# Kernel optimization log

Hardware: AMD Instinct MI355X
Metric: run time of the kernel (lower is better)

## Reference

```python
import jax, jax.numpy as jnp
import numpy as np

V = 50288; D = 768; L = 12; SPLIT = 6; L_LORA = L - SPLIT
NSTATE = 64; HDIM = 64
DIN = 2 * D                         # expand=2 -> 1536
H = DIN // HDIM                     # 24 heads
K = 4                               # depthwise conv kernel
DPROJ = 2 * DIN + 2 * NSTATE + H    # 3224
CONVD = DIN + 2 * NSTATE            # 1664
R = 8; LORA_SCALE = 2.0             # alpha/rank = 2r/r
EPS = 1e-5


def _rms(x, w):
    return x * jax.lax.rsqrt(jnp.mean(x * x, axis=-1, keepdims=True) + EPS) * w


def _ssm_scan(dt, A, Bm, Cm, xh):
    # dt:[B,T,H]  A:[H]  Bm,Cm:[B,T,N]  xh:[B,T,H,P]
    dA = jnp.exp(dt * A)
    def step(h, inp):
        dA_t, dt_t, B_t, C_t, x_t = inp
        h = dA_t[:, :, None, None] * h + (dt_t[..., None] * x_t)[..., None] * B_t[:, None, None, :]
        return h, jnp.einsum('bhpn,bn->bhp', h, C_t)
    h0 = jnp.zeros((dt.shape[0], H, HDIM, NSTATE), dt.dtype)
    xs = tuple(jnp.moveaxis(a, 1, 0) for a in (dA, dt, Bm, Cm, xh))
    _, ys = jax.lax.scan(step, h0, xs)
    return jnp.moveaxis(ys, 0, 1)  # [B,T,H,P]


@jax.checkpoint
def _mixer(u, in_w, cw, cb, dtb, A_log, Dsk, gw, out_w):
    # Mamba2 selective-scan block (ngroups=1, no biases on projections)
    Bsz, T, _ = u.shape
    zxbcdt = u @ in_w.T                              # [B,T,DPROJ]
    z = zxbcdt[..., :DIN]
    xBC = zxbcdt[..., DIN:DIN + CONVD]
    dt = zxbcdt[..., DIN + CONVD:]
    xp = jnp.pad(xBC, ((0, 0), (K - 1, 0), (0, 0)))  # causal depthwise conv1d
    xBC = jax.nn.silu(cb + sum(cw[:, k] * xp[:, k:k + T] for k in range(K)))
    xh = xBC[..., :DIN].reshape(Bsz, T, H, HDIM)
    Bm = xBC[..., DIN:DIN + NSTATE]
    Cm = xBC[..., DIN + NSTATE:]
    dt = jax.nn.softplus(dt + dtb)
    y = _ssm_scan(dt, -jnp.exp(A_log), Bm, Cm, xh) + Dsk[None, None, :, None] * xh
    y = _rms(y.reshape(Bsz, T, DIN) * jax.nn.silu(z), gw)   # gated RMSNorm
    return y @ out_w.T


def _run_base(x, res, p):
    def step(carry, q):
        x, res = carry
        res = x + res
        h = _mixer(_rms(res, q['nw']), q['iw'], q['cw'], q['cb'], q['dtb'],
                   q['al'], q['dk'], q['gw'], q['ow'])
        return (h, res), None
    (x, res), _ = jax.lax.scan(step, (x, res), p)
    return x, res


def _run_lora(x, res, p):
    def step(carry, q):
        x, res = carry
        res = x + res
        iw = q['iw'] + LORA_SCALE * (q['ibw'] @ q['iaw'])   # LoRALinear effective weight
        ow = q['ow'] + LORA_SCALE * (q['obw'] @ q['oaw'])
        h = _mixer(_rms(res, q['nw']), iw, q['cw'], q['cb'], q['dtb'],
                   q['al'], q['dk'], q['gw'], ow)
        return (h, res), None
    (x, res), _ = jax.lax.scan(step, (x, res), p)
    return x, res


def _rope(x, loop_i):
    # LoopRoPE: rotate interleaved pairs of hidden dims by angle theta_i * loop_i
    inv_freq = 1.0 / (10000.0 ** (jnp.arange(0, D, 2, dtype=jnp.float32) / D))
    f = loop_i * inv_freq
    cos_v = jnp.repeat(jnp.cos(f), 2)
    sin_v = jnp.repeat(jnp.sin(f), 2)
    x1, x2 = x[..., ::2], x[..., 1::2]
    rot = jnp.stack([-x2, x1], axis=-1).reshape(x.shape)
    return x * cos_v + rot * sin_v


def _forward(input_ids, n_loops, embedding, norm_w, in_w, conv_w, conv_b, dt_bias, A_log,
             D_skip, gnorm_w, out_w, lora_in_A, lora_in_B, lora_out_A, lora_out_B,
             core_in_w, core_conv_w, core_conv_b, core_dt_bias, core_A_log, core_D,
             core_gnorm_w, core_out_w, loop_norm_w, lifeline_gate, norm_f_w, lm_head_w):
    base = {'nw': norm_w[:SPLIT], 'iw': in_w[:SPLIT], 'cw': conv_w[:SPLIT], 'cb': conv_b[:SPLIT],
            'dtb': dt_bias[:SPLIT], 'al': A_log[:SPLIT], 'dk': D_skip[:SPLIT],
            'gw': gnorm_w[:SPLIT], 'ow': out_w[:SPLIT]}
    lora = {'nw': norm_w[SPLIT:], 'iw': in_w[SPLIT:], 'cw': conv_w[SPLIT:], 'cb': conv_b[SPLIT:],
            'dtb': dt_bias[SPLIT:], 'al': A_log[SPLIT:], 'dk': D_skip[SPLIT:],
            'gw': gnorm_w[SPLIT:], 'ow': out_w[SPLIT:],
            'iaw': lora_in_A, 'ibw': lora_in_B, 'oaw': lora_out_A, 'obw': lora_out_B}
    x = embedding[input_ids]                       # [B,T,D]
    res = jnp.zeros_like(x)                        # residual=None -> zeros
    x, res = _run_base(x, res, base)               # frozen layers [0:6]
    x, res = _run_lora(x, res, lora)               # LoRA layers [6:12]
    x_prompt = jax.lax.stop_gradient(x)            # x.clone().detach()
    for i in range(int(n_loops)):
        x = x + lifeline_gate * x_prompt           # lifeline injection
        x = _rope(x, float(i))                     # loop-index RoPE
        x, res = _run_lora(x, res, lora)           # run_lora recursion body
        x = x + _mixer(x, core_in_w, core_conv_w, core_conv_b, core_dt_bias,
                       core_A_log, core_D, core_gnorm_w, core_out_w)  # mamba2_core
        x = _rms(x, loop_norm_w)                   # loop_norm
    h = _rms(x + res, norm_f_w)                    # norm_f(x, residual, prenorm=False)
    return h @ lm_head_w.T                         # lm_head logits [B,T,V]


def setup_inputs() -> dict:
    key = jax.random.key(0)
    ks = iter(jax.random.split(key, 64))
    f32 = jnp.float32
    def w(shape, s=0.02):
        return (s * jax.random.normal(next(ks), shape)).astype(f32)
    inp = {
        'input_ids': jax.random.randint(next(ks), (2, 512), 0, 50277, dtype=jnp.int32),
        'n_loops': 3,
        'embedding': w((V, D)),
        'norm_w': jnp.ones((L, D), f32),
        'in_w': w((L, DPROJ, D)),
        'conv_w': w((L, CONVD, K), 0.2),
        'conv_b': jnp.zeros((L, CONVD), f32),
        'dt_bias': w((L, H), 0.5),
        'A_log': jnp.log(1.0 + 15.0 * jax.random.uniform(next(ks), (L, H))).astype(f32),
        'D_skip': jnp.ones((L, H), f32),
        'gnorm_w': jnp.ones((L, DIN), f32),
        'out_w': w((L, D, DIN)),
        'lora_in_A': w((L_LORA, R, D), 0.05),
        'lora_in_B': w((L_LORA, DPROJ, R), 0.05),
        'lora_out_A': w((L_LORA, R, DIN), 0.05),
        'lora_out_B': w((L_LORA, D, R), 0.05),
        'core_in_w': w((DPROJ, D)),
        'core_conv_w': w((CONVD, K), 0.2),
        'core_conv_b': jnp.zeros((CONVD,), f32),
        'core_dt_bias': w((H,), 0.5),
        'core_A_log': jnp.log(1.0 + 15.0 * jax.random.uniform(next(ks), (H,))).astype(f32),
        'core_D': jnp.ones((H,), f32),
        'core_gnorm_w': jnp.ones((DIN,), f32),
        'core_out_w': w((D, DIN)),
        'loop_norm_w': jnp.ones((D,), f32),
        'lifeline_gate': jnp.ones((D,), f32),
        'norm_f_w': jnp.ones((D,), f32),
        'lm_head_w': w((V, D)),
    }
    return inp


def reference(input_ids, n_loops, embedding, norm_w, in_w, conv_w, conv_b, dt_bias, A_log,
              D_skip, gnorm_w, out_w, lora_in_A, lora_in_B, lora_out_A, lora_out_B,
              core_in_w, core_conv_w, core_conv_b, core_dt_bias, core_A_log, core_D,
              core_gnorm_w, core_out_w, loop_norm_w, lifeline_gate, norm_f_w, lm_head_w):
    return _forward(input_ids, n_loops, embedding, norm_w, in_w, conv_w, conv_b, dt_bias,
                    A_log, D_skip, gnorm_w, out_w, lora_in_A, lora_in_B, lora_out_A,
                    lora_out_B, core_in_w, core_conv_w, core_conv_b, core_dt_bias,
                    core_A_log, core_D, core_gnorm_w, core_out_w, loop_norm_w,
                    lifeline_gate, norm_f_w, lm_head_w)
```

## Files before the change

kernel.cpp:

```cpp
#include <hip/hip_runtime.h>
#include <math.h>

constexpr int Bsz   = 2;
constexpr int Tseq  = 512;
constexpr int Mtok  = Bsz * Tseq;
constexpr int Dm    = 768;
constexpr int DINc  = 1536;
constexpr int Hn    = 24;
constexpr int NS    = 64;
constexpr int KC    = 4;
constexpr int DPROJc = 2*DINc + 2*NS + Hn;
constexpr int CONVDc = DINc + 2*NS;
constexpr int NL    = 12;
constexpr int SPL   = 6;
constexpr int LLO   = 6;
constexpr int NCH   = 8;
constexpr int Vv    = 50288;
constexpr float EPSc = 1e-5f;
constexpr int NLOOPS = 3;

#define DEVI __device__ __forceinline__

typedef _Float16 f16x8 __attribute__((ext_vector_type(8)));
typedef float    f32x4 __attribute__((ext_vector_type(4)));

DEVI float siluf(float x){ return x / (1.0f + expf(-x)); }
DEVI float softplusf(float x){ return (x > 20.0f) ? x : log1pf(expf(x)); }
DEVI unsigned short f2h(float f){
  union { _Float16 h; unsigned short u; } c;
  c.h = (_Float16)f;
  return c.u;
}
DEVI float h2f(unsigned short u){
  union { unsigned short u; _Float16 h; } c;
  c.u = u; return (float)c.h;
}

DEVI void gload16(const void* g, void* l){
  __builtin_amdgcn_global_load_lds(
      (const __attribute__((address_space(1))) void*)g,
      (__attribute__((address_space(3))) void*)l, 16, 0, 0);
}

DEVI float blk_reduce256(float v, float* sh){
  #pragma unroll
  for (int o = 32; o; o >>= 1) v += __shfl_down(v, o);
  int lane = threadIdx.x & 63, w = threadIdx.x >> 6;
  if (lane == 0) sh[w] = v;
  __syncthreads();
  return sh[0] + sh[1] + sh[2] + sh[3];
}

__global__ void k_embed(const int* __restrict__ ids, const float* __restrict__ emb,
                        float* __restrict__ x){
  int m = blockIdx.x;
  int id = ids[m];
  const float4* src = (const float4*)(emb + (size_t)id * Dm);
  float4* dst = (float4*)(x + (size_t)m * Dm);
  int i = threadIdx.x;
  dst[i] = src[i];
}

__global__ void k_f2h(const float* __restrict__ in, unsigned short* __restrict__ out, int n4){
  int e = blockIdx.x*256 + threadIdx.x;
  if (e >= n4) return;
  float4 v = ((const float4*)in)[e];
  ushort4 o; o.x=f2h(v.x); o.y=f2h(v.y); o.z=f2h(v.z); o.w=f2h(v.w);
  ((ushort4*)out)[e] = o;
}

__global__ __launch_bounds__(256) void k_addrms(const float* __restrict__ xin,
    float* __restrict__ res, unsigned short* __restrict__ ub,
    const float* __restrict__ w){
  int m = blockIdx.x, tid = threadIdx.x;
  __shared__ float sh[4];
  const float* xr = xin + (size_t)m*Dm;
  float* rr = res + (size_t)m*Dm;
  float r[3]; float ss = 0.f;
  #pragma unroll
  for (int k=0;k<3;k++){ int e = tid + k*256; float v = xr[e] + rr[e]; r[k]=v; ss += v*v; }
  ss = blk_reduce256(ss, sh);
  float rs = 1.0f / sqrtf(ss/(float)Dm + EPSc);
  #pragma unroll
  for (int k=0;k<3;k++){
    int e = tid + k*256;
    rr[e] = r[k];
    ub[(size_t)m*Dm+e] = f2h(r[k]*rs*w[e]);
  }
}

__global__ __launch_bounds__(256) void k_addrms_p(const float* __restrict__ part,
    float* __restrict__ res, unsigned short* __restrict__ ub,
    const float* __restrict__ w){
  int m = blockIdx.x, tid = threadIdx.x;
  __shared__ float sh[4];
  const size_t tot = (size_t)Mtok*Dm;
  float* rr = res + (size_t)m*Dm;
  float r[3]; float ss = 0.f;
  #pragma unroll
  for (int k=0;k<3;k++){
    int e = tid + k*256;
    size_t idx = (size_t)m*Dm + e;
    float v = rr[e] + part[idx] + part[tot+idx] + part[2*tot+idx] + part[3*tot+idx];
    r[k]=v; ss += v*v;
  }
  ss = blk_reduce256(ss, sh);
  float rs = 1.0f / sqrtf(ss/(float)Dm + EPSc);
  #pragma unroll
  for (int k=0;k<3;k++){
    int e = tid + k*256;
    rr[e] = r[k];
    ub[(size_t)m*Dm+e] = f2h(r[k]*rs*w[e]);
  }
}

__global__ void k_sum_xp(const float* __restrict__ part, float* __restrict__ x,
                         float* __restrict__ xp){
  size_t e = (size_t)blockIdx.x*256 + threadIdx.x;
  const size_t tot = (size_t)Mtok*Dm;
  if (e >= tot) return;
  float v = part[e] + part[tot+e] + part[2*tot+e] + part[3*tot+e];
  x[e] = v; xp[e] = v;
}

__global__ void k_f2h_sum(const float* __restrict__ part, float* __restrict__ x,
                          unsigned short* __restrict__ ub){
  size_t e = (size_t)blockIdx.x*256 + threadIdx.x;
  const size_t tot = (size_t)Mtok*Dm;
  if (e >= tot) return;
  float v = part[e] + part[tot+e] + part[2*tot+e] + part[3*tot+e];
  x[e] = v; ub[e] = f2h(v);
}

__global__ __launch_bounds__(256) void k_rms_p(const float* __restrict__ part,
    float* __restrict__ x, const float* __restrict__ w){
  int m = blockIdx.x, tid = threadIdx.x;
  __shared__ float sh[4];
  const size_t tot = (size_t)Mtok*Dm;
  float* xr = x + (size_t)m*Dm;
  float r[3]; float ss = 0.f;
  #pragma unroll
  for (int k=0;k<3;k++){
    int e = tid + k*256;
    size_t idx = (size_t)m*Dm + e;
    float v = xr[e] + part[idx] + part[tot+idx] + part[2*tot+idx] + part[3*tot+idx];
    r[k]=v; ss += v*v;
  }
  ss = blk_reduce256(ss, sh);
  float rs = 1.0f / sqrtf(ss/(float)Dm + EPSc);
  #pragma unroll
  for (int k=0;k<3;k++){ int e = tid + k*256; xr[e] = r[k]*rs*w[e]; }
}

__global__ __launch_bounds__(128) void k_liferope(float* __restrict__ x,
    const float* __restrict__ xp, const float* __restrict__ gate, float iF){
  int m = blockIdx.x, tid = threadIdx.x;
  float* xr = x + (size_t)m*Dm;
  const float* pr = xp + (size_t)m*Dm;
  #pragma unroll
  for (int k=0;k<3;k++){
    int j = tid + k*128;
    int d0 = 2*j, d1 = d0+1;
    float v0 = xr[d0] + gate[d0]*pr[d0];
    float v1 = xr[d1] + gate[d1]*pr[d1];
    float invf = expf(-9.210340371976184f * ((float)(2*j) * (1.0f/768.0f)));
    float f = iF * invf;
    float cv = cosf(f), sv = sinf(f);
    xr[d0] = v0*cv - v1*sv;
    xr[d1] = v1*cv + v0*sv;
  }
}

__global__ __launch_bounds__(256) void k_gemm_h(
    const unsigned short* __restrict__ A,
    const unsigned short* __restrict__ Bw,
    void* __restrict__ Cv, int Nd, int Kd, int outmode){
  alignas(16) __shared__ unsigned short lA[2][128*64];
  alignas(16) __shared__ unsigned short lB[2][128*64];
  const int tid  = threadIdx.x;
  const int lane = tid & 63;
  const int wv   = tid >> 6;
  const int wm   = wv >> 1, wn = wv & 1;
  const int gx = gridDim.x, gy = gridDim.y;
  const int nwg = gx*gy;
  const int flat = blockIdx.x + gx*blockIdx.y;
  const int q = nwg >> 3, r = nwg & 7;
  const int xcd = flat & 7, pos = flat >> 3;
  const int lg = (xcd < r ? xcd*(q+1) : r*(q+1) + (xcd - r)*q) + pos;
  const int m_idx = lg % gy, n_idx = lg / gy;
  const int n0 = n_idx * 128;
  const int m0 = m_idx * 128;
  const int KS = gridDim.z;
  const int kchunk = Kd / KS;
  const int kbeg = blockIdx.z * kchunk;
  const int nsteps = kchunk / 64;

  f32x4 acc[4][4] = {};

  auto stage = [&](int buf, int k0){
    #pragma unroll
    for (int i=0;i<4;i++){
      int seg = tid + i*256;
      int row = seg >> 3;
      int c8  = (seg & 7) ^ (row & 7);
      gload16(A + (size_t)(m0 + row)*Kd + k0 + c8*8, &lA[buf][seg*8]);
      int rn = n0 + row; rn = (rn < Nd) ? rn : (Nd - 1);
      gload16(Bw + (size_t)rn*Kd + k0 + c8*8, &lB[buf][seg*8]);
    }
  };

  stage(0, kbeg);
  for (int t=0; t<nsteps; ++t){
    const int cur = t & 1;
    if (t+1 < nsteps){
      stage(cur^1, kbeg + (t+1)*64);
      __builtin_amdgcn_sched_barrier(0);
      asm volatile("s_waitcnt vmcnt(8)" ::: "memory");
    } else {
      asm volatile("s_waitcnt vmcnt(0)" ::: "memory");
    }
    __builtin_amdgcn_s_barrier();
    __builtin_amdgcn_sched_barrier(0);
    #pragma unroll
    for (int kk=0; kk<2; kk++){
      f16x8 af[4], bfr[4];
      #pragma unroll
      for (int f=0; f<4; f++){
        int rowa = wm*64 + f*16 + (lane & 15);
        int ba = rowa*128 + ((kk*64 + (lane>>4)*16) ^ ((rowa & 7) << 4));
        af[f] = *(const f16x8*)((const char*)&lA[cur][0] + ba);
        int rowb = wn*64 + f*16 + (lane & 15);
        int bb = rowb*128 + ((kk*64 + (lane>>4)*16) ^ ((rowb & 7) << 4));
        bfr[f] = *(const f16x8*)((const char*)&lB[cur][0] + bb);
      }
      #pragma unroll
      for (int fm=0; fm<4; fm++)
        #pragma unroll
        for (int fn=0; fn<4; fn++)
          acc[fm][fn] = __builtin_amdgcn_mfma_f32_16x16x32_f16(af[fm], bfr[fn], acc[fm][fn], 0, 0, 0);
    }
    __builtin_amdgcn_s_barrier();
  }

  #pragma unroll
  for (int fm=0; fm<4; fm++){
    int mbase = m0 + wm*64 + fm*16 + ((lane>>4)<<2);
    #pragma unroll
    for (int fn=0; fn<4; fn++){
      int n = n0 + wn*64 + fn*16 + (lane & 15);
      if (n < Nd){
        #pragma unroll
        for (int rr=0;rr<4;rr++){
          size_t idx = (size_t)(mbase + rr)*Nd + n;
          float v = acc[fm][fn][rr];
          if (outmode == 0){
            float* Cb = (float*)Cv + (size_t)blockIdx.z*((size_t)Mtok*Nd);
            Cb[idx] = v;
          } else if (outmode == 1){
            ((float*)Cv)[idx] = v;
          } else {
            ((unsigned short*)Cv)[idx] = f2h(v);
          }
        }
      }
    }
  }
}

__global__ void k_prep_in(const float* __restrict__ W12, const float* __restrict__ Wc,
    const float* __restrict__ lA, const float* __restrict__ lB,
    unsigned short* __restrict__ out){
  const int tot4 = DPROJc*Dm/4;
  int e4 = blockIdx.x*256 + threadIdx.x;
  if (e4 >= tot4) return;
  int l = blockIdx.y;
  const float* W = (l < 12) ? W12 + (size_t)l*DPROJc*Dm : Wc;
  const int k4n = Dm/4;
  int n = e4 / k4n, k4 = e4 - n*k4n;
  float4 wv = *(const float4*)(W + (size_t)n*Dm + k4*4);
  float s0=wv.x, s1=wv.y, s2=wv.z, s3=wv.w;
  if (l >= SPL && l < 12){
    int ll = l - SPL;
    const float* Bl = lB + (size_t)ll*DPROJc*8;
    const float* Al = lA + (size_t)ll*8*Dm;
    #pragma unroll
    for (int r=0;r<8;r++){
      float b = 2.0f * Bl[n*8+r];
      float4 a = *(const float4*)(Al + (size_t)r*Dm + k4*4);
      s0 += b*a.x; s1 += b*a.y; s2 += b*a.z; s3 += b*a.w;
    }
  }
  ushort4 o; o.x=f2h(s0); o.y=f2h(s1); o.z=f2h(s2); o.w=f2h(s3);
  ((ushort4*)(out + (size_t)l*DPROJc*Dm))[e4] = o;
}

__global__ void k_prep_out(const float* __restrict__ W12, const float* __restrict__ Wc,
    const float* __restrict__ lA, const float* __restrict__ lB,
    unsigned short* __restrict__ out){
  const int tot4 = Dm*DINc/4;
  int e4 = blockIdx.x*256 + threadIdx.x;
  if (e4 >= tot4) return;
  int l = blockIdx.y;
  const float* W = (l < 12) ? W12 + (size_t)l*Dm*DINc : Wc;
  const int k4n = DINc/4;
  int n = e4 / k4n, k4 = e4 - n*k4n;
  float4 wv = *(const float4*)(W + (size_t)n*DINc + k4*4);
  float s0=wv.x, s1=wv.y, s2=wv.z, s3=wv.w;
  if (l >= SPL && l < 12){
    int ll = l - SPL;
    const float* Bl = lB + (size_t)ll*Dm*8;
    const float* Al = lA + (size_t)ll*8*DINc;
    #pragma unroll
    for (int r=0;r<8;r++){
      float b = 2.0f * Bl[n*8+r];
      float4 a = *(const float4*)(Al + (size_t)r*DINc + k4*4);
      s0 += b*a.x; s1 += b*a.y; s2 += b*a.z; s3 += b*a.w;
    }
  }
  ushort4 o; o.x=f2h(s0); o.y=f2h(s1); o.z=f2h(s2); o.w=f2h(s3);
  ((ushort4*)(out + (size_t)l*Dm*DINc))[e4] = o;
}

DEVI f16x8 ldfrag(const unsigned short (*T)[72], int row, int k0){
  return *(const f16x8*)&T[row][k0];
}

__global__ __launch_bounds__(256) void k_s1(const unsigned short* __restrict__ zxh,
    const float* __restrict__ cw, const float* __restrict__ cb,
    const float* __restrict__ dtb, const float* __restrict__ alog,
    float* __restrict__ S, float* __restrict__ ctot){
  int bh = blockIdx.x; int b = bh / Hn, h = bh % Hn; int c = blockIdx.y;
  __shared__ unsigned short XT[64][72];
  __shared__ unsigned short BwT[64][72];
  __shared__ float wv[64];
  int tid = threadIdx.x;
  int base_m = b*Tseq + c*64;
  if (tid < 64){
    float Av = -expf(alog[h]);
    float zdt = h2f(zxh[(size_t)(base_m+tid)*DPROJc + DINc + CONVDc + h]) + dtb[h];
    float dt = softplusf(zdt);
    float s = dt * Av;
    #pragma unroll
    for (int o=1;o<64;o<<=1){ float v = __shfl_up(s, o); if (tid >= o) s += v; }
    if (tid == 63) ctot[bh*NCH + c] = s;
    float ce = __shfl(s, 63);
    wv[tid] = expf(ce - s) * dt;
  }
  __syncthreads();
  int ch = tid & 63;
  int t0 = (tid >> 6) * 16;
  int tl = c*64 + t0;
  {
    int cc = h*64 + ch;
    float4 w4 = *(const float4*)&cw[cc*KC];
    float bias = cb[cc];
    const unsigned short* zp = zxh + (size_t)base_m*DPROJc + DINc + cc;
    float v0 = (tl >= 3) ? h2f(zp[(long)(t0-3)*DPROJc]) : 0.f;
    float v1 = (tl >= 2) ? h2f(zp[(long)(t0-2)*DPROJc]) : 0.f;
    float v2 = (tl >= 1) ? h2f(zp[(long)(t0-1)*DPROJc]) : 0.f;
    #pragma unroll
    for (int i=0;i<16;i++){
      float v3 = h2f(zp[(long)(t0+i)*DPROJc]);
      float o = bias + w4.x*v0 + w4.y*v1 + w4.z*v2 + w4.w*v3;
      XT[ch][t0+i] = f2h(siluf(o));
      v0=v1; v1=v2; v2=v3;
    }
  }
  {
    int cc = DINc + ch;
    float4 w4 = *(const float4*)&cw[cc*KC];
    float bias = cb[cc];
    const unsigned short* zp = zxh + (size_t)base_m*DPROJc + DINc + cc;
    float v0 = (tl >= 3) ? h2f(zp[(long)(t0-3)*DPROJc]) : 0.f;
    float v1 = (tl >= 2) ? h2f(zp[(long)(t0-2)*DPROJc]) : 0.f;
    float v2 = (tl >= 1) ? h2f(zp[(long)(t0-1)*DPROJc]) : 0.f;
    #pragma unroll
    for (int i=0;i<16;i++){
      float v3 = h2f(zp[(long)(t0+i)*DPROJc]);
      float o = bias + w4.x*v0 + w4.y*v1 + w4.z*v2 + w4.w*v3;
      BwT[ch][t0+i] = f2h(siluf(o) * wv[t0+i]);
      v0=v1; v1=v2; v2=v3;
    }
  }
  __syncthreads();
  int lane = tid & 63, wid = tid >> 6, wmp = wid >> 1, wnn = wid & 1;
  f32x4 acc[2][2] = {};
  #pragma unroll
  for (int kk=0; kk<2; kk++){
    int k0 = kk*32 + (lane>>4)*8;
    f16x8 a[2], bf[2];
    #pragma unroll
    for (int f=0; f<2; f++){
      a[f]  = ldfrag(XT,  wmp*32 + f*16 + (lane&15), k0);
      bf[f] = ldfrag(BwT, wnn*32 + f*16 + (lane&15), k0);
    }
    #pragma unroll
    for (int fm=0; fm<2; fm++)
      #pragma unroll
      for (int fn=0; fn<2; fn++)
        acc[fm][fn] = __builtin_amdgcn_mfma_f32_16x16x32_f16(a[fm], bf[fn], acc[fm][fn], 0, 0, 0);
  }
  float* Sb = S + ((size_t)(bh*NCH + c))*4096;
  #pragma unroll
  for (int fm=0; fm<2; fm++)
    #pragma unroll
    for (int fn=0; fn<2; fn++)
      #pragma unroll
      for (int rg=0; rg<4; rg++){
        int p = wmp*32 + fm*16 + ((lane>>4)<<2) + rg;
        int n = wnn*32 + fn*16 + (lane&15);
        Sb[p*64 + n] = acc[fm][fn][rg];
      }
}

__global__ void k_s2(const float* __restrict__ S, const float* __restrict__ ctot,
                     float* __restrict__ hst){
  int gid = blockIdx.x*256 + threadIdx.x;
  int bh = gid >> 12; int e = gid & 4095;
  float hv = 0.f;
  #pragma unroll
  for (int c=0;c<NCH;c++){
    size_t idx = ((size_t)(bh*NCH + c))*4096 + e;
    hst[idx] = hv;
    float Ac = expf(ctot[bh*NCH + c]);
    hv = Ac*hv + S[idx];
  }
}

__global__ __launch_bounds__(256) void k_s3(const unsigned short* __restrict__ zxh,
    const float* __restrict__ cw, const float* __restrict__ cb,
    const float* __restrict__ dtb, const float* __restrict__ alog,
    const float* __restrict__ hst, const float* __restrict__ Dsk,
    unsigned short* __restrict__ y){
  int bh = blockIdx.x; int b = bh / Hn, h = bh % Hn; int c = blockIdx.y;
  __shared__ unsigned short Ch[64][72];
  __shared__ unsigned short Bh[64][72];
  __shared__ unsigned short XhT[64][72];
  __shared__ unsigned short hT[64][72];
  __shared__ unsigned short Mh[64][72];
  __shared__ float cumS[64], dtS[64];
  int tid = threadIdx.x;
  int base_m = b*Tseq + c*64;
  if (tid < 64){
    float Av = -expf(alog[h]);
    float zdt = h2f(zxh[(size_t)(base_m+tid)*DPROJc + DINc + CONVDc + h]) + dtb[h];
    float dt = softplusf(zdt);
    float s = dt * Av;
    #pragma unroll
    for (int o=1;o<64;o<<=1){ float v = __shfl_up(s, o); if (tid >= o) s += v; }
    cumS[tid] = s;
    dtS[tid]  = dt;
  }
  int ch = tid & 63;
  int t0 = (tid >> 6) * 16;
  int tl = c*64 + t0;
  {
    int cc = h*64 + ch;
    float4 w4 = *(const float4*)&cw[cc*KC];
    float bias = cb[cc];
    const unsigned short* zp = zxh + (size_t)base_m*DPROJc + DINc + cc;
    float v0 = (tl >= 3) ? h2f(zp[(long)(t0-3)*DPROJc]) : 0.f;
    float v1 = (tl >= 2) ? h2f(zp[(long)(t0-2)*DPROJc]) : 0.f;
    float v2 = (tl >= 1) ? h2f(zp[(long)(t0-1)*DPROJc]) : 0.f;
    #pragma unroll
    for (int i=0;i<16;i++){
      float v3 = h2f(zp[(long)(t0+i)*DPROJc]);
      float o = bias + w4.x*v0 + w4.y*v1 + w4.z*v2 + w4.w*v3;
      XhT[ch][t0+i] = f2h(siluf(o));
      v0=v1; v1=v2; v2=v3;
    }
  }
  {
    int cc = DINc + ch;
    float4 w4 = *(const float4*)&cw[cc*KC];
    float bias = cb[cc];
    const unsigned short* zp = zxh + (size_t)base_m*DPROJc + DINc + cc;
    float v0 = (tl >= 3) ? h2f(zp[(long)(t0-3)*DPROJc]) : 0.f;
    float v1 = (tl >= 2) ? h2f(zp[(long)(t0-2)*DPROJc]) : 0.f;
    float v2 = (tl >= 1) ? h2f(zp[(long)(t0-1)*DPROJc]) : 0.f;
    #pragma unroll
    for (int i=0;i<16;i++){
      float v3 = h2f(zp[(long)(t0+i)*DPROJc]);
      float o = bias + w4.x*v0 + w4.y*v1 + w4.z*v2 + w4.w*v3;
      Bh[t0+i][ch] = f2h(siluf(o));
      v0=v1; v1=v2; v2=v3;
    }
  }
  {
    int cc = DINc + NS + ch;
    float4 w4 = *(const float4*)&cw[cc*KC];
    float bias = cb[cc];
    const unsigned short* zp = zxh + (size_t)base_m*DPROJc + DINc + cc;
    float v0 = (tl >= 3) ? h2f(zp[(long)(t0-3)*DPROJc]) : 0.f;
    float v1 = (tl >= 2) ? h2f(zp[(long)(t0-2)*DPROJc]) : 0.f;
    float v2 = (tl >= 1) ? h2f(zp[(long)(t0-1)*DPROJc]) : 0.f;
    #pragma unroll
    for (int i=0;i<16;i++){
      float v3 = h2f(zp[(long)(t0+i)*DPROJc]);
      float o = bias + w4.x*v0 + w4.y*v1 + w4.z*v2 + w4.w*v3;
      Ch[t0+i][ch] = f2h(siluf(o));
      v0=v1; v1=v2; v2=v3;
    }
  }
  {
    const float* hb = hst + ((size_t)(bh*NCH + c))*4096;
    for (int e4 = tid; e4 < 1024; e4 += 256){
      float4 hv = ((const float4*)hb)[e4];
      int p = (e4 << 2) >> 6, n = (e4 << 2) & 63;
      ushort4 o; o.x=f2h(hv.x); o.y=f2h(hv.y); o.z=f2h(hv.z); o.w=f2h(hv.w);
      *(ushort4*)&hT[p][n] = o;
    }
  }
  __syncthreads();
  int lane = tid & 63, wid = tid >> 6, wmt = wid >> 1, wns = wid & 1;
  f32x4 g[2][2] = {};
  #pragma unroll
  for (int kk=0; kk<2; kk++){
    int k0 = kk*32 + (lane>>4)*8;
    f16x8 a[2], bf[2];
    #pragma unroll
    for (int f=0; f<2; f++){
      a[f]  = ldfrag(Ch, wmt*32 + f*16 + (lane&15), k0);
      bf[f] = ldfrag(Bh, wns*32 + f*16 + (lane&15), k0);
    }
    #pragma unroll
    for (int fm=0; fm<2; fm++)
      #pragma unroll
      for (int fn=0; fn<2; fn++)
        g[fm][fn] = __builtin_amdgcn_mfma_f32_16x16x32_f16(a[fm], bf[fn], g[fm][fn], 0, 0, 0);
  }
  #pragma unroll
  for (int fm=0; fm<2; fm++)
    #pragma unroll
    for (int fn=0; fn<2; fn++)
      #pragma unroll
      for (int rg=0; rg<4; rg++){
        int t = wmt*32 + fm*16 + ((lane>>4)<<2) + rg;
        int s = wns*32 + fn*16 + (lane&15);
        float val = (s <= t) ? expf(cumS[t] - cumS[s]) * dtS[s] * g[fm][fn][rg] : 0.f;
        Mh[t][s] = f2h(val);
      }
  __syncthreads();
  f32x4 aL[2][2] = {}, aS[2][2] = {};
  #pragma unroll
  for (int kk=0; kk<2; kk++){
    int k0 = kk*32 + (lane>>4)*8;
    f16x8 m_[2], x_[2], c_[2], h_[2];
    #pragma unroll
    for (int f=0; f<2; f++){
      m_[f] = ldfrag(Mh,  wmt*32 + f*16 + (lane&15), k0);
      x_[f] = ldfrag(XhT, wns*32 + f*16 + (lane&15), k0);
      c_[f] = ldfrag(Ch,  wmt*32 + f*16 + (lane&15), k0);
      h_[f] = ldfrag(hT,  wns*32 + f*16 + (lane&15), k0);
    }
    #pragma unroll
    for (int fm=0; fm<2; fm++)
      #pragma unroll
      for (int fn=0; fn<2; fn++){
        aL[fm][fn] = __builtin_amdgcn_mfma_f32_16x16x32_f16(m_[fm], x_[fn], aL[fm][fn], 0, 0, 0);
        aS[fm][fn] = __builtin_amdgcn_mfma_f32_16x16x32_f16(c_[fm], h_[fn], aS[fm][fn], 0, 0, 0);
      }
  }
  float Dh = Dsk[h];
  #pragma unroll
  for (int fm=0; fm<2; fm++)
    #pragma unroll
    for (int fn=0; fn<2; fn++)
      #pragma unroll
      for (int rg=0; rg<4; rg++){
        int t = wmt*32 + fm*16 + ((lane>>4)<<2) + rg;
        int p = wns*32 + fn*16 + (lane&15);
        float Pt = expf(cumS[t]);
        float xv = h2f(XhT[p][t]);
        float o = aL[fm][fn][rg] + Pt*aS[fm][fn][rg] + Dh*xv;
        y[(size_t)(base_m+t)*DINc + h*64 + p] = f2h(o);
      }
}

__global__ __launch_bounds__(256) void k_gate(const unsigned short* __restrict__ zxh,
    const unsigned short* __restrict__ y, unsigned short* __restrict__ yb,
    const float* __restrict__ gw){
  int m = blockIdx.x, tid = threadIdx.x;
  __shared__ float sh[4];
  const unsigned short* zr = zxh + (size_t)m*DPROJc;
  const unsigned short* yr = y + (size_t)m*DINc;
  float g[6]; float ss = 0.f;
  #pragma unroll
  for (int k=0;k<6;k++){
    int e = tid + k*256;
    float z = h2f(zr[e]);
    float v = h2f(yr[e]) * siluf(z);
    g[k] = v; ss += v*v;
  }
  ss = blk_reduce256(ss, sh);
  float rs = 1.0f / sqrtf(ss/(float)DINc + EPSc);
  #pragma unroll
  for (int k=0;k<6;k++){
    int e = tid + k*256;
    yb[(size_t)m*DINc + e] = f2h(g[k]*rs*gw[e]);
  }
}

struct WSP {
  float *x,*res,*xp,*ctot,*Sc,*hst,*part;
  unsigned short *zxh,*yh,*ub,*yb,*wib,*wob,*whb;
};

static void run_mixer_h(hipStream_t st, const WSP& w, const unsigned short* ub_in,
    const unsigned short* iw, const float* cw, const float* cb, const float* dtb,
    const float* al, const float* dk, const float* gw, const unsigned short* ow){
  dim3 gIn((DPROJc + 127)/128, Mtok/128, 1);
  k_gemm_h<<<gIn, 256, 0, st>>>(ub_in, iw, w.zxh, DPROJc, Dm, 2);
  k_s1<<<dim3(Bsz*Hn, NCH), 256, 0, st>>>(w.zxh, cw, cb, dtb, al, w.Sc, w.ctot);
  k_s2<<<(Bsz*Hn*4096)/256, 256, 0, st>>>(w.Sc, w.ctot, w.hst);
  k_s3<<<dim3(Bsz*Hn, NCH), 256, 0, st>>>(w.zxh, cw, cb, dtb, al, w.hst, dk, w.yh);
  k_gate<<<Mtok, 256, 0, st>>>(w.zxh, w.yh, w.yb, gw);
  dim3 gOut(Dm/128, Mtok/128, 4);
  k_gemm_h<<<gOut, 256, 0, st>>>(w.yb, ow, w.part, Dm, DINc, 0);
}

extern "C" void kernel_launch(void* const* d_in, const int* in_sizes, int n_in,
                              void* d_out, int out_size, void* d_ws, size_t ws_size,
                              hipStream_t stream){
  const int*   ids        = (const int*)  d_in[0];
  const float* emb        = (const float*)d_in[2];
  const float* norm_w     = (const float*)d_in[3];
  const float* in_w       = (const float*)d_in[4];
  const float* conv_w     = (const float*)d_in[5];
  const float* conv_b     = (const float*)d_in[6];
  const float* dt_bias    = (const float*)d_in[7];
  const float* A_log      = (const float*)d_in[8];
  const float* D_skip     = (const float*)d_in[9];
  const float* gnorm_w    = (const float*)d_in[10];
  const float* out_w      = (const float*)d_in[11];
  const float* lora_in_A  = (const float*)d_in[12];
  const float* lora_in_B  = (const float*)d_in[13];
  const float* lora_out_A = (const float*)d_in[14];
  const float* lora_out_B = (const float*)d_in[15];
  const float* core_in_w  = (const float*)d_in[16];
  const float* core_conv_w= (const float*)d_in[17];
  const float* core_conv_b= (const float*)d_in[18];
  const float* core_dtb   = (const float*)d_in[19];
  const float* core_A_log = (const float*)d_in[20];
  const float* core_D     = (const float*)d_in[21];
  const float* core_gw    = (const float*)d_in[22];
  const float* core_out_w = (const float*)d_in[23];
  const float* loop_norm_w= (const float*)d_in[24];
  const float* life_gate  = (const float*)d_in[25];
  const float* norm_f_w   = (const float*)d_in[26];
  const float* lm_head_w  = (const float*)d_in[27];
  (void)in_sizes; (void)n_in; (void)out_size; (void)ws_size;

  char* pb = (char*)d_ws;
  auto balloc = [&](size_t bytes){
    char* q = pb; pb += (bytes + 255) & ~(size_t)255; return q;
  };
  WSP w;
  w.x    = (float*)balloc((size_t)Mtok*Dm*4);
  w.res  = (float*)balloc((size_t)Mtok*Dm*4);
  w.xp   = (float*)balloc((size_t)Mtok*Dm*4);
  w.ctot = (float*)balloc((size_t)Bsz*Hn*NCH*4);
  w.Sc   = (float*)balloc((size_t)Bsz*Hn*NCH*4096*4);
  w.hst  = (float*)balloc((size_t)Bsz*Hn*NCH*4096*4);
  w.part = (float*)balloc((size_t)4*Mtok*Dm*4);
  w.zxh  = (unsigned short*)balloc((size_t)Mtok*DPROJc*2);
  w.yh   = (unsigned short*)balloc((size_t)Mtok*DINc*2);
  w.ub   = (unsigned short*)balloc((size_t)Mtok*Dm*2);
  w.yb   = (unsigned short*)balloc((size_t)Mtok*DINc*2);

  const size_t IWN = (size_t)DPROJc*Dm;
  const size_t OWN = (size_t)Dm*DINc;
  const size_t HWN = (size_t)Vv*Dm;
  w.wib = (unsigned short*)balloc(13*IWN*2);
  w.wob = (unsigned short*)balloc(13*OWN*2);
  w.whb = (unsigned short*)balloc(HWN*2);

  k_prep_in<<<dim3((IWN/4 + 255)/256, 13), 256, 0, stream>>>(
      in_w, core_in_w, lora_in_A, lora_in_B, w.wib);
  k_prep_out<<<dim3((OWN/4 + 255)/256, 13), 256, 0, stream>>>(
      out_w, core_out_w, lora_out_A, lora_out_B, w.wob);
  k_f2h<<<(HWN/4 + 255)/256, 256, 0, stream>>>(lm_head_w, w.whb, (int)(HWN/4));

  k_embed<<<Mtok, 192, 0, stream>>>(ids, emb, w.x);
  hipMemsetAsync(w.res, 0, (size_t)Mtok*Dm*sizeof(float), stream);

  const size_t totMD = (size_t)Mtok*Dm;

  auto mixer_l = [&](int l){
    run_mixer_h(stream, w, w.ub,
        w.wib + (size_t)l*IWN, conv_w + (size_t)l*CONVDc*KC, conv_b + (size_t)l*CONVDc,
        dt_bias + (size_t)l*Hn, A_log + (size_t)l*Hn, D_skip + (size_t)l*Hn,
        gnorm_w + (size_t)l*DINc, w.wob + (size_t)l*OWN);
  };
  k_addrms<<<Mtok, 256, 0, stream>>>(w.x, w.res, w.ub, norm_w);
  mixer_l(0);
  for (int l=1; l<NL; l++){
    k_addrms_p<<<Mtok, 256, 0, stream>>>(w.part, w.res, w.ub, norm_w + (size_t)l*Dm);
    mixer_l(l);
  }
  k_sum_xp<<<(totMD + 255)/256, 256, 0, stream>>>(w.part, w.x, w.xp);
  for (int i=0;i<NLOOPS;i++){
    k_liferope<<<Mtok, 128, 0, stream>>>(w.x, w.xp, life_gate, (float)i);
    k_addrms<<<Mtok, 256, 0, stream>>>(w.x, w.res, w.ub, norm_w + (size_t)SPL*Dm);
    mixer_l(SPL);
    for (int l=SPL+1; l<NL; l++){
      k_addrms_p<<<Mtok, 256, 0, stream>>>(w.part, w.res, w.ub, norm_w + (size_t)l*Dm);
      mixer_l(l);
    }
    k_f2h_sum<<<(totMD + 255)/256, 256, 0, stream>>>(w.part, w.x, w.ub);
    run_mixer_h(stream, w, w.ub,
        w.wib + 12*IWN, core_conv_w, core_conv_b, core_dtb, core_A_log, core_D,
        core_gw, w.wob + 12*OWN);
    k_rms_p<<<Mtok, 256, 0, stream>>>(w.part, w.x, loop_norm_w);
  }
  k_addrms<<<Mtok, 256, 0, stream>>>(w.x, w.res, w.ub, norm_f_w);
  dim3 gHead((Vv + 127)/128, Mtok/128, 1);
  k_gemm_h<<<gHead, 256, 0, stream>>>(w.ub, w.whb, d_out, Vv, Dm, 1);
}
```

Before: 2.752 ms.

## Fuse gated RMSNorm into scan epilogue and out-projection GEMM

Removes the separate gating and RMSNorm kernel from each mixer. The scan kernel now applies the silu(z) gate, writes the gated output and atomically accumulates per-row sums of squares. The out-projection GEMM reads those sums and applies the inverse RMS scale in its epilogue, and the norm weight is folded into the pre-converted out_w columns. This saves a full read and write of the DIN-wide activation plus a kernel launch per mixer. In exchange it adds atomics, a buffer that earlier kernels must zero, and strided z loads inside the scan kernel.

```diff
diff --git a/kernel.cpp b/kernel.cpp
--- a/kernel.cpp
+++ b/kernel.cpp
@@ -71,7 +71,7 @@
 
 __global__ __launch_bounds__(256) void k_addrms(const float* __restrict__ xin,
     float* __restrict__ res, unsigned short* __restrict__ ub,
-    const float* __restrict__ w){
+    const float* __restrict__ w, float* __restrict__ rssum){
   int m = blockIdx.x, tid = threadIdx.x;
   __shared__ float sh[4];
   const float* xr = xin + (size_t)m*Dm;
@@ -80,6 +80,7 @@
   #pragma unroll
   for (int k=0;k<3;k++){ int e = tid + k*256; float v = xr[e] + rr[e]; r[k]=v; ss += v*v; }
   ss = blk_reduce256(ss, sh);
+  if (tid == 0 && rssum) rssum[m] = 0.f;
   float rs = 1.0f / sqrtf(ss/(float)Dm + EPSc);
   #pragma unroll
   for (int k=0;k<3;k++){
@@ -91,7 +92,7 @@
 
 __global__ __launch_bounds__(256) void k_addrms_p(const float* __restrict__ part,
     float* __restrict__ res, unsigned short* __restrict__ ub,
-    const float* __restrict__ w){
+    const float* __restrict__ w, float* __restrict__ rssum){
   int m = blockIdx.x, tid = threadIdx.x;
   __shared__ float sh[4];
   const size_t tot = (size_t)Mtok*Dm;
@@ -105,6 +106,7 @@
     r[k]=v; ss += v*v;
   }
   ss = blk_reduce256(ss, sh);
+  if (tid == 0 && rssum) rssum[m] = 0.f;
   float rs = 1.0f / sqrtf(ss/(float)Dm + EPSc);
   #pragma unroll
   for (int k=0;k<3;k++){
@@ -124,10 +126,11 @@
 }
 
 __global__ void k_f2h_sum(const float* __restrict__ part, float* __restrict__ x,
-                          unsigned short* __restrict__ ub){
+                          unsigned short* __restrict__ ub, float* __restrict__ rssum){
   size_t e = (size_t)blockIdx.x*256 + threadIdx.x;
   const size_t tot = (size_t)Mtok*Dm;
   if (e >= tot) return;
+  if (e < Mtok) rssum[e] = 0.f;
   float v = part[e] + part[tot+e] + part[2*tot+e] + part[3*tot+e];
   x[e] = v; ub[e] = f2h(v);
 }
@@ -174,9 +177,11 @@
 __global__ __launch_bounds__(256) void k_gemm_h(
     const unsigned short* __restrict__ A,
     const unsigned short* __restrict__ Bw,
-    void* __restrict__ Cv, int Nd, int Kd, int outmode){
+    void* __restrict__ Cv, int Nd, int Kd, int outmode,
+    const float* __restrict__ rsrow){
   alignas(16) __shared__ unsigned short lA[2][128*64];
   alignas(16) __shared__ unsigned short lB[2][128*64];
+  __shared__ float lRs[128];
   const int tid  = threadIdx.x;
   const int lane = tid & 63;
   const int wv   = tid >> 6;
@@ -195,6 +200,8 @@
   const int kbeg = blockIdx.z * kchunk;
   const int nsteps = kchunk / 64;
 
+  if (rsrow && tid < 128) lRs[tid] = rsrow[m0 + tid];
+
   f32x4 acc[4][4] = {};
 
   auto stage = [&](int buf, int k0){
@@ -244,7 +251,8 @@
 
   #pragma unroll
   for (int fm=0; fm<4; fm++){
-    int mbase = m0 + wm*64 + fm*16 + ((lane>>4)<<2);
+    int mloc = wm*64 + fm*16 + ((lane>>4)<<2);
+    int mbase = m0 + mloc;
     #pragma unroll
     for (int fn=0; fn<4; fn++){
       int n = n0 + wn*64 + fn*16 + (lane & 15);
@@ -253,6 +261,8 @@
         for (int rr=0;rr<4;rr++){
           size_t idx = (size_t)(mbase + rr)*Nd + n;
           float v = acc[fm][fn][rr];
+          if (rsrow)
+            v *= 1.0f / sqrtf(lRs[mloc + rr]*(1.0f/(float)DINc) + EPSc);
           if (outmode == 0){
             float* Cb = (float*)Cv + (size_t)blockIdx.z*((size_t)Mtok*Nd);
             Cb[idx] = v;
@@ -296,12 +306,14 @@
 
 __global__ void k_prep_out(const float* __restrict__ W12, const float* __restrict__ Wc,
     const float* __restrict__ lA, const float* __restrict__ lB,
+    const float* __restrict__ gnw, const float* __restrict__ core_gw,
     unsigned short* __restrict__ out){
   const int tot4 = Dm*DINc/4;
   int e4 = blockIdx.x*256 + threadIdx.x;
   if (e4 >= tot4) return;
   int l = blockIdx.y;
   const float* W = (l < 12) ? W12 + (size_t)l*Dm*DINc : Wc;
+  const float* gw = (l < 12) ? gnw + (size_t)l*DINc : core_gw;
   const int k4n = DINc/4;
   int n = e4 / k4n, k4 = e4 - n*k4n;
   float4 wv = *(const float4*)(W + (size_t)n*DINc + k4*4);
@@ -317,6 +329,8 @@
       s0 += b*a.x; s1 += b*a.y; s2 += b*a.z; s3 += b*a.w;
     }
   }
+  float4 g4 = *(const float4*)(gw + k4*4);
+  s0 *= g4.x; s1 *= g4.y; s2 *= g4.z; s3 *= g4.w;
   ushort4 o; o.x=f2h(s0); o.y=f2h(s1); o.z=f2h(s2); o.w=f2h(s3);
   ((ushort4*)(out + (size_t)l*Dm*DINc))[e4] = o;
 }
@@ -431,7 +445,7 @@
     const float* __restrict__ cw, const float* __restrict__ cb,
     const float* __restrict__ dtb, const float* __restrict__ alog,
     const float* __restrict__ hst, const float* __restrict__ Dsk,
-    unsigned short* __restrict__ y){
+    unsigned short* __restrict__ g_out, float* __restrict__ rssum){
   int bh = blockIdx.x; int b = bh / Hn, h = bh % Hn; int c = blockIdx.y;
   __shared__ unsigned short Ch[64][72];
   __shared__ unsigned short Bh[64][72];
@@ -563,60 +577,45 @@
   }
   float Dh = Dsk[h];
   #pragma unroll
-  for (int fm=0; fm<2; fm++)
-    #pragma unroll
-    for (int fn=0; fn<2; fn++)
+  for (int fm=0; fm<2; fm++){
+    #pragma unroll
+    for (int rg=0; rg<4; rg++){
+      int t = wmt*32 + fm*16 + ((lane>>4)<<2) + rg;
+      float Pt = expf(cumS[t]);
+      float sq = 0.f;
       #pragma unroll
-      for (int rg=0; rg<4; rg++){
-        int t = wmt*32 + fm*16 + ((lane>>4)<<2) + rg;
+      for (int fn=0; fn<2; fn++){
         int p = wns*32 + fn*16 + (lane&15);
-        float Pt = expf(cumS[t]);
         float xv = h2f(XhT[p][t]);
-        float o = aL[fm][fn][rg] + Pt*aS[fm][fn][rg] + Dh*xv;
-        y[(size_t)(base_m+t)*DINc + h*64 + p] = f2h(o);
+        float yv = aL[fm][fn][rg] + Pt*aS[fm][fn][rg] + Dh*xv;
+        float z = h2f(zxh[(size_t)(base_m+t)*DPROJc + h*64 + p]);
+        float gv = yv * siluf(z);
+        g_out[(size_t)(base_m+t)*DINc + h*64 + p] = f2h(gv);
+        sq += gv*gv;
       }
-}
-
-__global__ __launch_bounds__(256) void k_gate(const unsigned short* __restrict__ zxh,
-    const unsigned short* __restrict__ y, unsigned short* __restrict__ yb,
-    const float* __restrict__ gw){
-  int m = blockIdx.x, tid = threadIdx.x;
-  __shared__ float sh[4];
-  const unsigned short* zr = zxh + (size_t)m*DPROJc;
-  const unsigned short* yr = y + (size_t)m*DINc;
-  float g[6]; float ss = 0.f;
-  #pragma unroll
-  for (int k=0;k<6;k++){
-    int e = tid + k*256;
-    float z = h2f(zr[e]);
-    float v = h2f(yr[e]) * siluf(z);
-    g[k] = v; ss += v*v;
-  }
-  ss = blk_reduce256(ss, sh);
-  float rs = 1.0f / sqrtf(ss/(float)DINc + EPSc);
-  #pragma unroll
-  for (int k=0;k<6;k++){
-    int e = tid + k*256;
-    yb[(size_t)m*DINc + e] = f2h(g[k]*rs*gw[e]);
+      sq += __shfl_xor(sq, 1); sq += __shfl_xor(sq, 2);
+      sq += __shfl_xor(sq, 4); sq += __shfl_xor(sq, 8);
+      if ((lane & 15) == 0) atomicAdd(&rssum[base_m + t], sq);
+    }
   }
 }
 
 struct WSP {
-  float *x,*res,*xp,*ctot,*Sc,*hst,*part;
-  unsigned short *zxh,*yh,*ub,*yb,*wib,*wob,*whb;
+  float *x,*res,*xp,*ctot,*Sc,*hst,*part,*rssum;
+  unsigned short *zxh,*ub,*yb,*wib,*wob,*whb;
 };
 
 static void run_mixer_h(hipStream_t st, const WSP& w, const unsigned short* ub_in,
     const unsigned short* iw, const float* cw, const float* cb, const float* dtb,
-    const float* al, const float* dk, const float* gw, const unsigned short* ow){
+    const float* al, const float* dk, const unsigned short* ow){
   dim3 gIn((DPROJc + 127)/128, Mtok/128, 1);
-  k_gemm_h<<<gIn, 256, 0, st>>>(ub_in, iw, w.zxh, DPROJc, Dm, 2);
+  k_gemm_h<<<gIn, 256, 0, st>>>(ub_in, iw, w.zxh, DPROJc, Dm, 2, nullptr);
   k_s1<<<dim3(Bsz*Hn, NCH), 256, 0, st>>>(w.zxh, cw, cb, dtb, al, w.Sc, w.ctot);
   k_s2<<<(Bsz*Hn*4096)/256, 256, 0, st>>>(w.Sc, w.ctot, w.hst);
-  k_s3<<<dim3(Bsz*Hn, NCH), 256, 0, st>>>(w.zxh, cw, cb, dtb, al, w.hst, dk, w.yh);
-  k_gate<<<Mtok, 256, 0, st>>>(w.zxh, w.yh, w.yb, gw);
+  k_s3<<<dim3(Bsz*Hn, NCH), 256, 0, st>>>(w.zxh, cw, cb, dtb, al, w.hst, dk,
+                                           w.yb, w.rssum);
   dim3 gOut(Dm/128, Mtok/128, 4);
-  k_gemm_h<<<gOut, 256, 0, st>>>(w.yb, ow, w.part, Dm, DINc, 0);
+  k_gemm_h<<<gOut, 256, 0, st>>>(w.yb, ow, w.part, Dm, DINc, 0, w.rssum);
 }
 
 extern "C" void kernel_launch(void* const* d_in, const int* in_sizes, int n_in,
@@ -656,17 +655,17 @@
     char* q = pb; pb += (bytes + 255) & ~(size_t)255; return q;
   };
   WSP w;
-  w.x    = (float*)balloc((size_t)Mtok*Dm*4);
-  w.res  = (float*)balloc((size_t)Mtok*Dm*4);
-  w.xp   = (float*)balloc((size_t)Mtok*Dm*4);
-  w.ctot = (float*)balloc((size_t)Bsz*Hn*NCH*4);
-  w.Sc   = (float*)balloc((size_t)Bsz*Hn*NCH*4096*4);
-  w.hst  = (float*)balloc((size_t)Bsz*Hn*NCH*4096*4);
-  w.part = (float*)balloc((size_t)4*Mtok*Dm*4);
-  w.zxh  = (unsigned short*)balloc((size_t)Mtok*DPROJc*2);
-  w.yh   = (unsigned short*)balloc((size_t)Mtok*DINc*2);
-  w.ub   = (unsigned short*)balloc((size_t)Mtok*Dm*2);
-  w.yb   = (unsigned short*)balloc((size_t)Mtok*DINc*2);
+  w.x     = (float*)balloc((size_t)Mtok*Dm*4);
+  w.res   = (float*)balloc((size_t)Mtok*Dm*4);
+  w.xp    = (float*)balloc((size_t)Mtok*Dm*4);
+  w.ctot  = (float*)balloc((size_t)Bsz*Hn*NCH*4);
+  w.Sc    = (float*)balloc((size_t)Bsz*Hn*NCH*4096*4);
+  w.hst   = (float*)balloc((size_t)Bsz*Hn*NCH*4096*4);
+  w.part  = (float*)balloc((size_t)4*Mtok*Dm*4);
+  w.rssum = (float*)balloc((size_t)Mtok*4);
+  w.zxh   = (unsigned short*)balloc((size_t)Mtok*DPROJc*2);
+  w.ub    = (unsigned short*)balloc((size_t)Mtok*Dm*2);
+  w.yb    = (unsigned short*)balloc((size_t)Mtok*DINc*2);
 
   const size_t IWN = (size_t)DPROJc*Dm;
   const size_t OWN = (size_t)Dm*DINc;
@@ -678,7 +677,7 @@
   k_prep_in<<<dim3((IWN/4 + 255)/256, 13), 256, 0, stream>>>(
       in_w, core_in_w, lora_in_A, lora_in_B, w.wib);
   k_prep_out<<<dim3((OWN/4 + 255)/256, 13), 256, 0, stream>>>(
-      out_w, core_out_w, lora_out_A, lora_out_B, w.wob);
+      out_w, core_out_w, lora_out_A, lora_out_B, gnorm_w, core_gw, w.wob);
   k_f2h<<<(HWN/4 + 255)/256, 256, 0, stream>>>(lm_head_w, w.whb, (int)(HWN/4));
 
   k_embed<<<Mtok, 192, 0, stream>>>(ids, emb, w.x);
@@ -690,30 +689,30 @@
     run_mixer_h(stream, w, w.ub,
         w.wib + (size_t)l*IWN, conv_w + (size_t)l*CONVDc*KC, conv_b + (size_t)l*CONVDc,
         dt_bias + (size_t)l*Hn, A_log + (size_t)l*Hn, D_skip + (size_t)l*Hn,
-        gnorm_w + (size_t)l*DINc, w.wob + (size_t)l*OWN);
+        w.wob + (size_t)l*OWN);
   };
-  k_addrms<<<Mtok, 256, 0, stream>>>(w.x, w.res, w.ub, norm_w);
+  k_addrms<<<Mtok, 256, 0, stream>>>(w.x, w.res, w.ub, norm_w, w.rssum);
   mixer_l(0);
   for (int l=1; l<NL; l++){
-    k_addrms_p<<<Mtok, 256, 0, stream>>>(w.part, w.res, w.ub, norm_w + (size_t)l*Dm);
+    k_addrms_p<<<Mtok, 256, 0, stream>>>(w.part, w.res, w.ub, norm_w + (size_t)l*Dm, w.rssum);
     mixer_l(l);
   }
   k_sum_xp<<<(totMD + 255)/256, 256, 0, stream>>>(w.part, w.x, w.xp);
   for (int i=0;i<NLOOPS;i++){
     k_liferope<<<Mtok, 128, 0, stream>>>(w.x, w.xp, life_gate, (float)i);
-    k_addrms<<<Mtok, 256, 0, stream>>>(w.x, w.res, w.ub, norm_w + (size_t)SPL*Dm);
+    k_addrms<<<Mtok, 256, 0, stream>>>(w.x, w.res, w.ub, norm_w + (size_t)SPL*Dm, w.rssum);
     mixer_l(SPL);
     for (int l=SPL+1; l<NL; l++){
-      k_addrms_p<<<Mtok, 256, 0, stream>>>(w.part, w.res, w.ub, norm_w + (size_t)l*Dm);
+      k_addrms_p<<<Mtok, 256, 0, stream>>>(w.part, w.res, w.ub, norm_w + (size_t)l*Dm, w.rssum);
       mixer_l(l);
     }
-    k_f2h_sum<<<(totMD + 255)/256, 256, 0, stream>>>(w.part, w.x, w.ub);
+    k_f2h_sum<<<(totMD + 255)/256, 256, 0, stream>>>(w.part, w.x, w.ub, w.rssum);
     run_mixer_h(stream, w, w.ub,
         w.wib + 12*IWN, core_conv_w, core_conv_b, core_dtb, core_A_log, core_D,
-        core_gw, w.wob + 12*OWN);
+        w.wob + 12*OWN);
     k_rms_p<<<Mtok, 256, 0, stream>>>(w.part, w.x, loop_norm_w);
   }
-  k_addrms<<<Mtok, 256, 0, stream>>>(w.x, w.res, w.ub, norm_f_w);
+  k_addrms<<<Mtok, 256, 0, stream>>>(w.x, w.res, w.ub, norm_f_w, nullptr);
   dim3 gHead((Vv + 127)/128, Mtok/128, 1);
-  k_gemm_h<<<gHead, 256, 0, stream>>>(w.ub, w.whb, d_out, Vv, Dm, 1);
-}
+  k_gemm_h<<<gHead, 256, 0, stream>>>(w.ub, w.whb, d_out, Vv, Dm, 1, nullptr);
+}
```

After: 3.143 ms. 1.14x slower.

## Fuse inter-chunk state recurrence into chunk output kernel, removing k_s2

Applied to the files above, without the earlier changes.

Drops the separate chunk-state scan kernel and its hst buffer. Each k_s3 block now rebuilds its starting state directly as a decay-weighted sum of all earlier chunks' states, with the weights computed from ctot in shared memory. This saves one launch per mixer and the hst write/read round trip, but turns the sequential scan into redundant O(c) reads of S per chunk, which adds global traffic to later chunks and load imbalance across blocks.

```diff
diff --git a/kernel.cpp b/kernel.cpp
--- a/kernel.cpp
+++ b/kernel.cpp
@@ -413,25 +413,11 @@
       }
 }
 
-__global__ void k_s2(const float* __restrict__ S, const float* __restrict__ ctot,
-                     float* __restrict__ hst){
-  int gid = blockIdx.x*256 + threadIdx.x;
-  int bh = gid >> 12; int e = gid & 4095;
-  float hv = 0.f;
-  #pragma unroll
-  for (int c=0;c<NCH;c++){
-    size_t idx = ((size_t)(bh*NCH + c))*4096 + e;
-    hst[idx] = hv;
-    float Ac = expf(ctot[bh*NCH + c]);
-    hv = Ac*hv + S[idx];
-  }
-}
-
 __global__ __launch_bounds__(256) void k_s3(const unsigned short* __restrict__ zxh,
     const float* __restrict__ cw, const float* __restrict__ cb,
     const float* __restrict__ dtb, const float* __restrict__ alog,
-    const float* __restrict__ hst, const float* __restrict__ Dsk,
-    unsigned short* __restrict__ y){
+    const float* __restrict__ Sg, const float* __restrict__ ctot,
+    const float* __restrict__ Dsk, unsigned short* __restrict__ y){
   int bh = blockIdx.x; int b = bh / Hn, h = bh % Hn; int c = blockIdx.y;
   __shared__ unsigned short Ch[64][72];
   __shared__ unsigned short Bh[64][72];
@@ -439,6 +425,7 @@
   __shared__ unsigned short hT[64][72];
   __shared__ unsigned short Mh[64][72];
   __shared__ float cumS[64], dtS[64];
+  __shared__ float wch[NCH];
   int tid = threadIdx.x;
   int base_m = b*Tseq + c*64;
   if (tid < 64){
@@ -450,6 +437,12 @@
     for (int o=1;o<64;o<<=1){ float v = __shfl_up(s, o); if (tid >= o) s += v; }
     cumS[tid] = s;
     dtS[tid]  = dt;
+  }
+  if (tid >= 64 && tid < 64 + NCH){
+    int cp = tid - 64;
+    float s = 0.f;
+    for (int j = cp+1; j < c; ++j) s += ctot[bh*NCH + j];
+    wch[cp] = (cp < c) ? expf(s) : 0.f;
   }
   int ch = tid & 63;
   int t0 = (tid >> 6) * 16;
@@ -502,15 +495,6 @@
       v0=v1; v1=v2; v2=v3;
     }
   }
-  {
-    const float* hb = hst + ((size_t)(bh*NCH + c))*4096;
-    for (int e4 = tid; e4 < 1024; e4 += 256){
-      float4 hv = ((const float4*)hb)[e4];
-      int p = (e4 << 2) >> 6, n = (e4 << 2) & 63;
-      ushort4 o; o.x=f2h(hv.x); o.y=f2h(hv.y); o.z=f2h(hv.z); o.w=f2h(hv.w);
-      *(ushort4*)&hT[p][n] = o;
-    }
-  }
   __syncthreads();
   int lane = tid & 63, wid = tid >> 6, wmt = wid >> 1, wns = wid & 1;
   f32x4 g[2][2] = {};
@@ -540,6 +524,20 @@
         float val = (s <= t) ? expf(cumS[t] - cumS[s]) * dtS[s] * g[fm][fn][rg] : 0.f;
         Mh[t][s] = f2h(val);
       }
+  {
+    const float* Sb0 = Sg + ((size_t)bh*NCH)*4096;
+    for (int e4 = tid; e4 < 1024; e4 += 256){
+      float a0=0.f, a1=0.f, a2=0.f, a3=0.f;
+      for (int cp = 0; cp < c; ++cp){
+        float wv = wch[cp];
+        float4 sv = ((const float4*)(Sb0 + (size_t)cp*4096))[e4];
+        a0 += wv*sv.x; a1 += wv*sv.y; a2 += wv*sv.z; a3 += wv*sv.w;
+      }
+      int p = (e4 << 2) >> 6, n = (e4 << 2) & 63;
+      ushort4 o; o.x=f2h(a0); o.y=f2h(a1); o.z=f2h(a2); o.w=f2h(a3);
+      *(ushort4*)&hT[p][n] = o;
+    }
+  }
   __syncthreads();
   f32x4 aL[2][2] = {}, aS[2][2] = {};
   #pragma unroll
@@ -602,7 +600,7 @@
 }
 
 struct WSP {
-  float *x,*res,*xp,*ctot,*Sc,*hst,*part;
+  float *x,*res,*xp,*ctot,*Sc,*part;
   unsigned short *zxh,*yh,*ub,*yb,*wib,*wob,*whb;
 };
 
@@ -612,8 +610,8 @@
   dim3 gIn((DPROJc + 127)/128, Mtok/128, 1);
   k_gemm_h<<<gIn, 256, 0, st>>>(ub_in, iw, w.zxh, DPROJc, Dm, 2);
   k_s1<<<dim3(Bsz*Hn, NCH), 256, 0, st>>>(w.zxh, cw, cb, dtb, al, w.Sc, w.ctot);
-  k_s2<<<(Bsz*Hn*4096)/256, 256, 0, st>>>(w.Sc, w.ctot, w.hst);
-  k_s3<<<dim3(Bsz*Hn, NCH), 256, 0, st>>>(w.zxh, cw, cb, dtb, al, w.hst, dk, w.yh);
+  k_s3<<<dim3(Bsz*Hn, NCH), 256, 0, st>>>(w.zxh, cw, cb, dtb, al, w.Sc, w.ctot,
+                                           dk, w.yh);
   k_gate<<<Mtok, 256, 0, st>>>(w.zxh, w.yh, w.yb, gw);
   dim3 gOut(Dm/128, Mtok/128, 4);
   k_gemm_h<<<gOut, 256, 0, st>>>(w.yb, ow, w.part, Dm, DINc, 0);
@@ -661,7 +659,6 @@
   w.xp   = (float*)balloc((size_t)Mtok*Dm*4);
   w.ctot = (float*)balloc((size_t)Bsz*Hn*NCH*4);
   w.Sc   = (float*)balloc((size_t)Bsz*Hn*NCH*4096*4);
-  w.hst  = (float*)balloc((size_t)Bsz*Hn*NCH*4096*4);
   w.part = (float*)balloc((size_t)4*Mtok*Dm*4);
   w.zxh  = (unsigned short*)balloc((size_t)Mtok*DPROJc*2);
   w.yh   = (unsigned short*)balloc((size_t)Mtok*DINc*2);
```

Measured after the change: 2.776 ms. About the same (+0.9%).
